# Performance work log

Hardware: AMD Instinct MI355X
Metric: run time of the kernel (lower is better)

The kernel has to match this reference:

```python
import jax, jax.numpy as jnp
import numpy as np

IN_F, OUT_F, HID_UNITS = 768, 4, 2048
H = (HID_UNITS // 16) * OUT_F          # 512
H_STANCE, OUT_S = 1024, 4
T, BR, L = 64, 4, 6                    # trees, branching factor, levels


def _build_forest():
    counts = np.array([BR ** (L - 1 - o) for o in range(L)])   # nodes per level, leaves (order 0) first
    starts = np.concatenate([[0], np.cumsum(counts)[:-1]])
    npt = int(counts.sum())                                    # 1365 nodes per tree
    offsets = np.arange(T) * npt
    node_order = np.tile(np.repeat(np.arange(L), counts), T)
    adj, eord = [], []
    for o in range(1, L):
        p = starts[o] + np.repeat(np.arange(counts[o]), BR)    # parents sorted, BR children each
        ch = starts[o - 1] + np.arange(counts[o - 1])
        pg = (offsets[:, None] + p[None, :]).reshape(-1)       # globally sorted parents per level
        cg = (offsets[:, None] + ch[None, :]).reshape(-1)
        adj.append(np.stack([pg, cg], 1))
        eord.append(np.full(pg.shape[0], o))
    return (node_order.astype(np.int32),
            np.concatenate(adj, 0).astype(np.int32),
            np.concatenate(eord).astype(np.int32),
            (offsets + starts[L - 1]).astype(np.int32),
            T * npt)


def setup_inputs():
    node_order, adjacency_list, edge_order, root_node, N = _build_forest()
    key = jax.random.key(0)
    ks = jax.random.split(key, 10)

    def xav(k, shape):
        lim = float(np.sqrt(6.0 / (shape[0] + shape[1])))
        return jax.random.uniform(k, shape, jnp.float32, -lim, lim)

    return {
        "features": jax.random.normal(ks[0], (N, IN_F), jnp.float32),
        "node_order": jnp.asarray(node_order),
        "adjacency_list": jnp.asarray(adjacency_list),
        "edge_order": jnp.asarray(edge_order),
        "root_node": jnp.asarray(root_node),
        "root_label": jax.random.randint(ks[1], (T,), 0, OUT_F, jnp.int32),
        "W_iou": xav(ks[2], (3 * H, IN_F)),
        "b_iou": jnp.zeros((3 * H,), jnp.float32),
        "U_iou": xav(ks[3], (3 * H, H)),
        "W_f": xav(ks[4], (H, IN_F)),
        "b_f": jnp.zeros((H,), jnp.float32),
        "U_f": xav(ks[5], (H, H)),
        "W_ff": xav(ks[6], (OUT_F, H)),
        "W_sd": xav(ks[7], (H_STANCE, H)),
        "W_sd2": xav(ks[8], (H, H_STANCE)),
        "W_sf": xav(ks[9], (OUT_S, H)),
        "ln_gamma": jnp.ones((OUT_S,), jnp.float32),
        "ln_beta": jnp.zeros((OUT_S,), jnp.float32),
    }


def _tree_lstm(features, node_order, adjacency_list, edge_order, root_node,
               W_iou, b_iou, U_iou, W_f, b_f, U_f,
               W_ff, W_sd, W_sd2, W_sf, ln_gamma, ln_beta):
    node_order = np.asarray(node_order)
    edge_order = np.asarray(edge_order)
    adjacency_list = np.asarray(adjacency_list)
    root_node = np.asarray(root_node)
    N = features.shape[0]
    Hd = W_f.shape[0]
    h = jnp.zeros((N, Hd), features.dtype)
    c = jnp.zeros((N, Hd), features.dtype)
    for n in range(int(node_order.max()) + 1):
        idx = np.nonzero(node_order == n)[0]           # nodes evaluated at this level (sorted)
        x = features[idx]
        if n == 0:
            iou = x @ W_iou.T + b_iou
            i, o, u = jnp.split(iou, 3, axis=1)
            c_new = jax.nn.sigmoid(i) * jnp.tanh(u)
        else:
            e = adjacency_list[edge_order == n]
            par, chi = e[:, 0], e[:, 1]                # parents grouped + sorted (unique_consecutive)
            seg = np.searchsorted(idx, par)            # parent id -> row within this level's block
            child_h = h[chi]
            child_c = c[chi]
            h_sum = jax.ops.segment_sum(child_h, seg, num_segments=idx.shape[0])
            iou = x @ W_iou.T + b_iou + h_sum @ U_iou.T
            i, o, u = jnp.split(iou, 3, axis=1)
            f = jax.nn.sigmoid(features[par] @ W_f.T + b_f + child_h @ U_f.T)
            c_sum = jax.ops.segment_sum(f * child_c, seg, num_segments=idx.shape[0])
            c_new = jax.nn.sigmoid(i) * jnp.tanh(u) + c_sum
        h_new = jax.nn.sigmoid(o) * jnp.tanh(c_new)
        c = c.at[idx].set(c_new)
        h = h.at[idx].set(h_new)
    residual = h
    h_root = h[root_node] @ W_ff.T
    h_st = (h @ W_sd.T) @ W_sd2.T + residual           # dropout = identity (eval mode)
    h_st = h_st @ W_sf.T
    mu = jnp.mean(h_st, axis=-1, keepdims=True)
    var = jnp.var(h_st, axis=-1, keepdims=True)
    h_st = (h_st - mu) * jax.lax.rsqrt(var + 1e-6) * ln_gamma + ln_beta
    return jax.nn.softmax(h_st, axis=1), jax.nn.softmax(h_root, axis=1), c


def reference(features, node_order, adjacency_list, edge_order, root_node, root_label,
              W_iou, b_iou, U_iou, W_f, b_f, U_f, W_ff, W_sd, W_sd2, W_sf, ln_gamma, ln_beta):
    return _tree_lstm(features, node_order, adjacency_list, edge_order, root_node,
                      W_iou, b_iou, U_iou, W_f, b_f, U_f,
                      W_ff, W_sd, W_sd2, W_sf, ln_gamma, ln_beta)
```

## Files before the change

kernel.cpp:

```cpp
#include <hip/hip_runtime.h>
#include <hip/hip_bf16.h>
#include <math.h>

typedef _Float16 f16;
typedef f16 f16x8 __attribute__((ext_vector_type(8)));
typedef float f32x4 __attribute__((ext_vector_type(4)));

#define NPT 1365
#define HD 512
#define NINT 341
#define IOU_LDS (2*128*64*2 + 2*192*64*2)
#define G128_LDS (2*128*64*2 + 2*128*64*2)

__device__ __forceinline__ float frcp(float x){ return __builtin_amdgcn_rcpf(x); }
__device__ __forceinline__ float sigm(float x){ return frcp(1.0f+__expf(-x)); }
__device__ __forceinline__ float ftanh(float x){
  float e=__expf(2.f*fabsf(x));
  float t=1.f-2.f*frcp(e+1.f);
  return copysignf(t,x);
}

__device__ __forceinline__ void gll16(const void* g, void* l){
  __builtin_amdgcn_global_load_lds((const __attribute__((address_space(1))) void*)g,
                                   (__attribute__((address_space(3))) void*)l, 16, 0, 0);
}

__device__ __forceinline__ void xcd_map(int phys, int nb, int xdim, int& x, int& my){
  int ytiles = nb / xdim;
  if((ytiles & 7)==0){
    int k = phys & 7, i = phys >> 3;
    my = k * (ytiles >> 3) + i / xdim;
    x  = i % xdim;
  }else{
    x  = phys % xdim;
    my = phys / xdim;
  }
}

__global__ void k_cvt16(const float* __restrict__ s, f16* __restrict__ d, size_t n8){
  size_t i=(size_t)blockIdx.x*blockDim.x+threadIdx.x;
  if(i>=n8) return;
  const float4* sp=(const float4*)(s+i*8);
  float4 a=sp[0], b=sp[1];
  float v[8]={a.x,a.y,a.z,a.w,b.x,b.y,b.z,b.w};
  f16x8 h;
  #pragma unroll
  for(int e=0;e<8;++e) h[e]=(f16)v[e];
  *(f16x8*)(d+i*8)=h;
}

__global__ void k_wil(const float* __restrict__ W, const float* __restrict__ U,
                      f16* __restrict__ d, int internal){
  const int K = internal? 1280 : 768;
  size_t i=(size_t)blockIdx.x*blockDim.x+threadIdx.x;
  size_t tot=(size_t)1536*K;
  if(i>=tot) return;
  int rp=(int)(i/K); int k=(int)(i-(size_t)rp*K);
  int f=rp>>4, rr=rp&15;
  int g=f%3, cgrp=f/3;
  int orig=g*512+cgrp*16+rr;
  float v;
  if(internal) v = (k<768)? W[(size_t)orig*768+k] : U[(size_t)orig*512+(k-768)];
  else         v = W[(size_t)orig*768+k];
  d[i]=(f16)v;
}

__global__ void k_concat1280(const float* __restrict__ W, const float* __restrict__ U,
                             f16* __restrict__ d, int rows){
  size_t i=(size_t)blockIdx.x*blockDim.x+threadIdx.x;
  const int K=1280;
  size_t tot=(size_t)rows*K;
  if(i>=tot) return;
  int r=(int)(i/K); int k=(int)(i-(size_t)r*K);
  float v = (k<768)? W[(size_t)r*768+k] : U[(size_t)r*512+(k-768)];
  d[i]=(f16)v;
}

__global__ void k_tmp4(const float* __restrict__ Wsf, const float* __restrict__ Wsd2,
                       float* __restrict__ tmp){
  int idx=blockIdx.x*256+threadIdx.x;
  if(idx>=4096) return;
  int j=idx>>10, e=idx&1023;
  float s=0.f;
  #pragma unroll 8
  for(int d=0;d<512;++d) s+=Wsf[j*512+d]*Wsd2[(size_t)d*1024+e];
  tmp[(size_t)j*1024+e]=s;
}

__global__ void k_wy2(const float* __restrict__ Wsf, const float* __restrict__ tmp,
                      const float* __restrict__ Wsd, float* __restrict__ Wy){
  int idx=blockIdx.x*256+threadIdx.x;
  if(idx>=2048) return;
  int j=idx>>9, c=idx&511;
  float s=Wsf[j*512+c];
  #pragma unroll 8
  for(int e=0;e<1024;++e) s+=tmp[j*1024+e]*Wsd[(size_t)e*512+c];
  Wy[(size_t)j*512+c]=s;
}

__global__ __launch_bounds__(256,2)
void k_iou128p(const f16* __restrict__ fx, const f16* __restrict__ hs16,
               const f16* __restrict__ Wil, const float* __restrict__ bias,
               const float* __restrict__ csum, f16* __restrict__ h16,
               float* __restrict__ cbuf,
               int start_n, int shift, int internal)
{
  extern __shared__ char sm[];
  char* Abase=sm;
  char* Bbase=sm+32768;
  const int tid=threadIdx.x;
  const int w=tid>>6, lane=tid&63;
  int x, my;
  xcd_map(blockIdx.x, gridDim.x, 8, x, my);
  const int m0=my*128;
  const int K = internal? 1280 : 768;
  const int NT = K>>6;

  unsigned fofs[4], hofs[4];
  #pragma unroll
  for(int i=0;i<4;++i){
    int r=w*32+i*8+(lane>>3);
    int m=m0+r;
    int t_=m>>shift, j=m-(t_<<shift);
    fofs[i]=(unsigned)(((size_t)t_*NPT+start_n+j)*768);
    hofs[i]=(unsigned)m*512u;
  }
  unsigned bofs[6];
  #pragma unroll
  for(int i=0;i<6;++i){
    int r=x*192+w*48+i*8+(lane>>3);
    bofs[i]=(unsigned)r*(unsigned)K;
  }
  const unsigned swz=8u*((unsigned)(lane&7)^(unsigned)(lane>>3));

  f32x4 acc[4][6];
  #pragma unroll
  for(int mi=0;mi<4;++mi)
    #pragma unroll
    for(int ni=0;ni<6;++ni) acc[mi][ni]=(f32x4){0.f,0.f,0.f,0.f};

  const int wr=(w>>1)*64;
  const int wcF=(w&1)*6;
  const int lr=lane&15, lg=lane>>4;

  auto STAGE=[&](int buf, int t){
    const f16* base; int kt; bool useF;
    if(internal){
      if(t<12){ base=fx;   kt=t;    useF=true;  }
      else    { base=hs16; kt=t-12; useF=false; }
    }else{
      base=fx; kt=t; useF=true;
    }
    const unsigned kofs=(unsigned)kt*64u+swz;
    char* Ad=Abase+(size_t)buf*16384;
    #pragma unroll
    for(int i=0;i<4;++i){
      const f16* g=base+(useF?fofs[i]:hofs[i])+kofs;
      gll16(g, Ad+(w*32+i*8)*128);
    }
    const unsigned bk=(unsigned)t*64u+swz;
    char* Bd=Bbase+(size_t)buf*24576;
    #pragma unroll
    for(int i=0;i<6;++i){
      gll16(Wil+bofs[i]+bk, Bd+(w*48+i*8)*128);
    }
  };

  auto COMPUTE=[&](int cur){
    const char* Ab=Abase+(size_t)cur*16384;
    const char* Bb=Bbase+(size_t)cur*24576;
    #pragma unroll
    for(int ks=0;ks<2;++ks){
      const unsigned cb=((unsigned)(ks*64+lg*16)) ^ ((unsigned)(lr&7)<<4);
      f16x8 av[4], bv[6];
      #pragma unroll
      for(int mi=0;mi<4;++mi)
        av[mi]=*(const f16x8*)(Ab+(unsigned)(wr+mi*16+lr)*128u+cb);
      #pragma unroll
      for(int ni=0;ni<6;++ni)
        bv[ni]=*(const f16x8*)(Bb+(unsigned)((wcF+ni)*16+lr)*128u+cb);
      __builtin_amdgcn_s_setprio(1);
      #pragma unroll
      for(int ni=0;ni<6;++ni)
        #pragma unroll
        for(int mi=0;mi<4;++mi)
          acc[mi][ni]=__builtin_amdgcn_mfma_f32_16x16x32_f16(av[mi],bv[ni],acc[mi][ni],0,0,0);
      __builtin_amdgcn_s_setprio(0);
    }
  };

  STAGE(0,0);
  STAGE(1,1);
  asm volatile("s_waitcnt vmcnt(10)" ::: "memory");
  __builtin_amdgcn_s_barrier();
  __builtin_amdgcn_sched_barrier(0);

  for(int t=0;t<NT;++t){
    COMPUTE(t&1);
    if(t+1<NT){
      __builtin_amdgcn_sched_barrier(0);
      __builtin_amdgcn_s_barrier();
      __builtin_amdgcn_sched_barrier(0);
      if(t+2<NT){
        STAGE(t&1, t+2);
        asm volatile("s_waitcnt vmcnt(10)" ::: "memory");
      }else{
        asm volatile("s_waitcnt vmcnt(0)" ::: "memory");
      }
      __builtin_amdgcn_s_barrier();
      __builtin_amdgcn_sched_barrier(0);
    }
  }

  #pragma unroll
  for(int mi=0;mi<4;++mi){
    #pragma unroll
    for(int cg=0;cg<2;++cg){
      const int col = x*64 + ((w&1)*2+cg)*16 + lr;
      const float bi=bias[col], bo=bias[col+512], bu=bias[col+1024];
      #pragma unroll
      for(int r=0;r<4;++r){
        const int mm=m0+wr+mi*16+lg*4+r;
        float iv=acc[mi][3*cg+0][r]+bi;
        float ov=acc[mi][3*cg+1][r]+bo;
        float uv=acc[mi][3*cg+2][r]+bu;
        float cn=sigm(iv)*ftanh(uv);
        if(internal) cn+=csum[(size_t)mm*HD+col];
        float hn=sigm(ov)*ftanh(cn);
        const int tt=mm>>shift, jj=mm-(tt<<shift);
        const size_t nd=((size_t)tt*NPT+start_n+jj)*HD+col;
        cbuf[nd]=cn;
        h16[nd]=(f16)hn;
      }
    }
  }
}

__global__ __launch_bounds__(256)
void k_iou(const f16* __restrict__ fx, const f16* __restrict__ hs16,
           const f16* __restrict__ Wcat, const float* __restrict__ bias,
           const float* __restrict__ csum, f16* __restrict__ h16,
           float* __restrict__ cbuf,
           int start_n, int shift, int K, int KB, int internal)
{
  __shared__ f16 As[64][40];
  __shared__ f16 Bs[3][64][40];
  const int tid=threadIdx.x;
  const int m0=blockIdx.x*64, n0=blockIdx.y*64;
  const int srow=tid>>2, skc=(tid&3)*8;
  const int m=m0+srow;
  const int t=m>>shift, j=m-(t<<shift);
  const size_t frow=((size_t)t*NPT+start_n+j)*768;
  const f16* aF=fx+frow;
  const f16* aH=hs16+(size_t)m*HD;
  const f16* bp0=Wcat+(size_t)(n0+srow)*KB;
  const f16* bp1=Wcat+(size_t)(512+n0+srow)*KB;
  const f16* bp2=Wcat+(size_t)(1024+n0+srow)*KB;

  f32x4 acc[3][2][2];
  #pragma unroll
  for(int g=0;g<3;++g)
    #pragma unroll
    for(int mi=0;mi<2;++mi)
      #pragma unroll
      for(int ni=0;ni<2;++ni) acc[g][mi][ni]=(f32x4){0.f,0.f,0.f,0.f};

  const int w=tid>>6, lane=tid&63;
  const int wr=(w>>1)*32, wc=(w&1)*32;
  const int lr=lane&15, lg=lane>>4;

  for(int k0=0;k0<K;k0+=32){
    const f16* ap = (k0<768)? (aF+k0) : (aH+(k0-768));
    *(f16x8*)&As[srow][skc]=*(const f16x8*)(ap+skc);
    *(f16x8*)&Bs[0][srow][skc]=*(const f16x8*)(bp0+k0+skc);
    *(f16x8*)&Bs[1][srow][skc]=*(const f16x8*)(bp1+k0+skc);
    *(f16x8*)&Bs[2][srow][skc]=*(const f16x8*)(bp2+k0+skc);
    __syncthreads();
    f16x8 a0=*(f16x8*)&As[wr+lr][lg*8];
    f16x8 a1=*(f16x8*)&As[wr+16+lr][lg*8];
    #pragma unroll
    for(int g=0;g<3;++g){
      #pragma unroll
      for(int ni=0;ni<2;++ni){
        f16x8 bv=*(f16x8*)&Bs[g][wc+ni*16+lr][lg*8];
        acc[g][0][ni]=__builtin_amdgcn_mfma_f32_16x16x32_f16(a0,bv,acc[g][0][ni],0,0,0);
        acc[g][1][ni]=__builtin_amdgcn_mfma_f32_16x16x32_f16(a1,bv,acc[g][1][ni],0,0,0);
      }
    }
    __syncthreads();
  }

  #pragma unroll
  for(int mi=0;mi<2;++mi){
    #pragma unroll
    for(int ni=0;ni<2;++ni){
      const int col=n0+wc+ni*16+lr;
      const float bi=bias[col], bo=bias[col+512], bu=bias[col+1024];
      #pragma unroll
      for(int r=0;r<4;++r){
        const int mm=m0+wr+mi*16+lg*4+r;
        float iv=acc[0][mi][ni][r]+bi;
        float ov=acc[1][mi][ni][r]+bo;
        float uv=acc[2][mi][ni][r]+bu;
        float cn=sigm(iv)*ftanh(uv);
        if(internal) cn+=csum[(size_t)mm*HD+col];
        float hn=sigm(ov)*ftanh(cn);
        const int tt=mm>>shift, jj=mm-(tt<<shift);
        const size_t nd=((size_t)tt*NPT+start_n+jj)*HD+col;
        cbuf[nd]=cn;
        h16[nd]=(f16)hn;
      }
    }
  }
}

__global__ __launch_bounds__(256,2)
void k_xwf128p(const f16* __restrict__ fx,
               const f16* __restrict__ Wfc, float* __restrict__ XWf, int Mtot)
{
  extern __shared__ char sm[];
  char* Abase=sm;
  char* Bbase=sm+32768;
  const int tid=threadIdx.x;
  const int w=tid>>6, lane=tid&63;
  int xb, my;
  xcd_map(blockIdx.x, gridDim.x, 4, xb, my);
  const int m0=my*128, n0=xb*128;
  const int NT=12;

  unsigned fofs[4];
  #pragma unroll
  for(int i=0;i<4;++i){
    int r=w*32+i*8+(lane>>3);
    int m=m0+r; if(m>=Mtot) m=Mtot-1;
    int t=m/NINT; int j=1024+(m-t*NINT);
    fofs[i]=(unsigned)(((size_t)t*NPT+j)*768);
  }
  unsigned bofs[4];
  #pragma unroll
  for(int i=0;i<4;++i){
    int r=n0+w*32+i*8+(lane>>3);
    bofs[i]=(unsigned)r*768u;
  }
  const unsigned swz=8u*((unsigned)(lane&7)^(unsigned)(lane>>3));

  f32x4 acc[4][4];
  #pragma unroll
  for(int mi=0;mi<4;++mi)
    #pragma unroll
    for(int ni=0;ni<4;++ni) acc[mi][ni]=(f32x4){0.f,0.f,0.f,0.f};

  const int wr=(w>>1)*64, wc=(w&1)*64;
  const int lr=lane&15, lg=lane>>4;

  auto STAGE=[&](int buf, int t){
    const unsigned ak=(unsigned)t*64u, bk=(unsigned)t*64u;
    char* Ad=Abase+(size_t)buf*16384;
    #pragma unroll
    for(int i=0;i<4;++i)
      gll16(fx+fofs[i]+ak+swz, Ad+(w*32+i*8)*128);
    char* Bd=Bbase+(size_t)buf*16384;
    #pragma unroll
    for(int i=0;i<4;++i)
      gll16(Wfc+bofs[i]+bk+swz, Bd+(w*32+i*8)*128);
  };

  auto COMPUTE=[&](int cur){
    const char* Ab=Abase+(size_t)cur*16384;
    const char* Bb=Bbase+(size_t)cur*16384;
    #pragma unroll
    for(int ks=0;ks<2;++ks){
      const unsigned cb=((unsigned)(ks*64+lg*16)) ^ ((unsigned)(lr&7)<<4);
      f16x8 av[4], bv[4];
      #pragma unroll
      for(int mi=0;mi<4;++mi)
        av[mi]=*(const f16x8*)(Ab+(unsigned)(wr+mi*16+lr)*128u+cb);
      #pragma unroll
      for(int ni=0;ni<4;++ni)
        bv[ni]=*(const f16x8*)(Bb+(unsigned)((wc+ni*16)+lr)*128u+cb);
      __builtin_amdgcn_s_setprio(1);
      #pragma unroll
      for(int ni=0;ni<4;++ni)
        #pragma unroll
        for(int mi=0;mi<4;++mi)
          acc[mi][ni]=__builtin_amdgcn_mfma_f32_16x16x32_f16(av[mi],bv[ni],acc[mi][ni],0,0,0);
      __builtin_amdgcn_s_setprio(0);
    }
  };

  STAGE(0,0);
  STAGE(1,1);
  asm volatile("s_waitcnt vmcnt(8)" ::: "memory");
  __builtin_amdgcn_s_barrier();
  __builtin_amdgcn_sched_barrier(0);

  for(int t=0;t<NT;++t){
    COMPUTE(t&1);
    if(t+1<NT){
      __builtin_amdgcn_sched_barrier(0);
      __builtin_amdgcn_s_barrier();
      __builtin_amdgcn_sched_barrier(0);
      if(t+2<NT){
        STAGE(t&1, t+2);
        asm volatile("s_waitcnt vmcnt(8)" ::: "memory");
      }else{
        asm volatile("s_waitcnt vmcnt(0)" ::: "memory");
      }
      __builtin_amdgcn_s_barrier();
      __builtin_amdgcn_sched_barrier(0);
    }
  }

  #pragma unroll
  for(int mi=0;mi<4;++mi){
    #pragma unroll
    for(int ni=0;ni<4;++ni){
      const int col=n0+wc+ni*16+lr;
      #pragma unroll
      for(int r=0;r<4;++r){
        const int mm=m0+wr+mi*16+lg*4+r;
        if(mm<Mtot) XWf[(size_t)mm*512+col]=acc[mi][ni][r];
      }
    }
  }
}

__global__ __launch_bounds__(256,2)
void k_uh128p(const f16* __restrict__ h16,
              const f16* __restrict__ Ufc, const float* __restrict__ bias,
              const float* __restrict__ XWf, const float* __restrict__ cbuf,
              float* __restrict__ csum, f16* __restrict__ hs16,
              int start_ch, int lc, int xwoff)
{
  extern __shared__ char sm[];
  char* Abase=sm;
  char* Bbase=sm+32768;
  const int tid=threadIdx.x;
  const int w=tid>>6, lane=tid&63;
  int xb, my;
  xcd_map(blockIdx.x, gridDim.x, 4, xb, my);
  const int e0=my*128, n0=xb*128;
  const int NT=8;

  unsigned hofs[4];
  #pragma unroll
  for(int i=0;i<4;++i){
    int r=w*32+i*8+(lane>>3);
    int e=e0+r;
    int t=e>>lc, ei=e-(t<<lc);
    hofs[i]=(unsigned)(((size_t)t*NPT+start_ch+ei)*HD);
  }
  unsigned bofs[4];
  #pragma unroll
  for(int i=0;i<4;++i){
    int r=n0+w*32+i*8+(lane>>3);
    bofs[i]=(unsigned)r*512u;
  }
  const unsigned swz=8u*((unsigned)(lane&7)^(unsigned)(lane>>3));

  f32x4 acc[4][4];
  #pragma unroll
  for(int mi=0;mi<4;++mi)
    #pragma unroll
    for(int ni=0;ni<4;++ni) acc[mi][ni]=(f32x4){0.f,0.f,0.f,0.f};

  const int wr=(w>>1)*64, wc=(w&1)*64;
  const int lr=lane&15, lg=lane>>4;

  auto STAGE=[&](int buf, int t){
    const unsigned ak=(unsigned)t*64u, bk=(unsigned)t*64u;
    char* Ad=Abase+(size_t)buf*16384;
    #pragma unroll
    for(int i=0;i<4;++i)
      gll16(h16+hofs[i]+ak+swz, Ad+(w*32+i*8)*128);
    char* Bd=Bbase+(size_t)buf*16384;
    #pragma unroll
    for(int i=0;i<4;++i)
      gll16(Ufc+bofs[i]+bk+swz, Bd+(w*32+i*8)*128);
  };

  auto COMPUTE=[&](int cur){
    const char* Ab=Abase+(size_t)cur*16384;
    const char* Bb=Bbase+(size_t)cur*16384;
    #pragma unroll
    for(int ks=0;ks<2;++ks){
      const unsigned cb=((unsigned)(ks*64+lg*16)) ^ ((unsigned)(lr&7)<<4);
      f16x8 av[4], bv[4];
      #pragma unroll
      for(int mi=0;mi<4;++mi)
        av[mi]=*(const f16x8*)(Ab+(unsigned)(wr+mi*16+lr)*128u+cb);
      #pragma unroll
      for(int ni=0;ni<4;++ni)
        bv[ni]=*(const f16x8*)(Bb+(unsigned)((wc+ni*16)+lr)*128u+cb);
      __builtin_amdgcn_s_setprio(1);
      #pragma unroll
      for(int ni=0;ni<4;++ni)
        #pragma unroll
        for(int mi=0;mi<4;++mi)
          acc[mi][ni]=__builtin_amdgcn_mfma_f32_16x16x32_f16(av[mi],bv[ni],acc[mi][ni],0,0,0);
      __builtin_amdgcn_s_setprio(0);
    }
  };

  STAGE(0,0);
  STAGE(1,1);
  asm volatile("s_waitcnt vmcnt(8)" ::: "memory");
  __builtin_amdgcn_s_barrier();
  __builtin_amdgcn_sched_barrier(0);

  for(int t=0;t<NT;++t){
    COMPUTE(t&1);
    if(t+1<NT){
      __builtin_amdgcn_sched_barrier(0);
      __builtin_amdgcn_s_barrier();
      __builtin_amdgcn_sched_barrier(0);
      if(t+2<NT){
        STAGE(t&1, t+2);
        asm volatile("s_waitcnt vmcnt(8)" ::: "memory");
      }else{
        asm volatile("s_waitcnt vmcnt(0)" ::: "memory");
      }
      __builtin_amdgcn_s_barrier();
      __builtin_amdgcn_sched_barrier(0);
    }
  }

  #pragma unroll
  for(int mi=0;mi<4;++mi){
    const int ebase=e0+wr+mi*16+lg*4;
    const int tt=ebase>>lc, eib=ebase-(tt<<lc);
    const int inode=tt*NINT + xwoff + (eib>>2);
    const int par=ebase>>2;
    #pragma unroll
    for(int ni=0;ni<4;++ni){
      const int col=n0+wc+ni*16+lr;
      const float base=bias[col]+XWf[(size_t)inode*512+col];
      const size_t chbase=((size_t)tt*NPT+start_ch+eib)*HD+col;
      float s=0.f, hsv=0.f;
      #pragma unroll
      for(int r=0;r<4;++r){
        const size_t ci=chbase+(size_t)r*HD;
        float fv=sigm(acc[mi][ni][r]+base);
        s+=fv*cbuf[ci];
        hsv+=(float)h16[ci];
      }
      csum[(size_t)par*HD+col]=s;
      hs16[(size_t)par*HD+col]=(f16)hsv;
    }
  }
}

__global__ __launch_bounds__(256)
void k_final2(const f16* __restrict__ h16,
              const float* __restrict__ Wy, const float* __restrict__ gamma,
              const float* __restrict__ beta, float* __restrict__ out0, int Nn)
{
  const int gtid=blockIdx.x*256+threadIdx.x;
  const int node=gtid>>6, lane=gtid&63;
  if(node>=Nn) return;
  const size_t base=(size_t)node*HD+lane*8;
  f16x8 hv=*(const f16x8*)(h16+base);
  float hf[8];
  #pragma unroll
  for(int e=0;e<8;++e) hf[e]=(float)hv[e];
  float y[4];
  #pragma unroll
  for(int jj=0;jj<4;++jj){
    const float* wp=Wy+jj*HD+lane*8;
    float s=0.f;
    #pragma unroll
    for(int e=0;e<8;++e) s+=hf[e]*wp[e];
    #pragma unroll
    for(int off=32;off>=1;off>>=1) s+=__shfl_xor(s,off,64);
    y[jj]=s;
  }
  if(lane==0){
    float mu=0.25f*(y[0]+y[1]+y[2]+y[3]);
    float var=0.f;
    #pragma unroll
    for(int jj=0;jj<4;++jj){ float d=y[jj]-mu; var+=d*d; }
    var*=0.25f;
    float rs=rsqrtf(var+1e-6f);
    float z[4], zmax=-1e30f;
    #pragma unroll
    for(int jj=0;jj<4;++jj){ z[jj]=(y[jj]-mu)*rs*gamma[jj]+beta[jj]; zmax=fmaxf(zmax,z[jj]); }
    float es=0.f;
    #pragma unroll
    for(int jj=0;jj<4;++jj){ z[jj]=__expf(z[jj]-zmax); es+=z[jj]; }
    float inv=1.f/es;
    #pragma unroll
    for(int jj=0;jj<4;++jj) out0[(size_t)node*4+jj]=z[jj]*inv;
  }
}

__global__ __launch_bounds__(256)
void k_root(const f16* __restrict__ h16,
            const float* __restrict__ Wff, float* __restrict__ out1)
{
  const int gtid=blockIdx.x*256+threadIdx.x;
  const int tt=gtid>>6, lane=gtid&63;
  if(tt>=64) return;
  const size_t base=((size_t)tt*NPT+1364)*HD+lane*8;
  f16x8 hv=*(const f16x8*)(h16+base);
  float hf[8];
  #pragma unroll
  for(int e=0;e<8;++e) hf[e]=(float)hv[e];
  float y[4];
  #pragma unroll
  for(int jj=0;jj<4;++jj){
    const float* wp=Wff+jj*HD+lane*8;
    float s=0.f;
    #pragma unroll
    for(int e=0;e<8;++e) s+=hf[e]*wp[e];
    #pragma unroll
    for(int off=32;off>=1;off>>=1) s+=__shfl_xor(s,off,64);
    y[jj]=s;
  }
  if(lane==0){
    float zmax=fmaxf(fmaxf(y[0],y[1]),fmaxf(y[2],y[3]));
    float es=0.f, z[4];
    #pragma unroll
    for(int jj=0;jj<4;++jj){ z[jj]=__expf(y[jj]-zmax); es+=z[jj]; }
    float inv=1.f/es;
    #pragma unroll
    for(int jj=0;jj<4;++jj) out1[(size_t)tt*4+jj]=z[jj]*inv;
  }
}

extern "C" void kernel_launch(void* const* d_in, const int* in_sizes, int n_in,
                              void* d_out, int out_size, void* d_ws, size_t ws_size,
                              hipStream_t stream)
{
  const float* features=(const float*)d_in[0];
  const float* W_iou=(const float*)d_in[6];
  const float* b_iou=(const float*)d_in[7];
  const float* U_iou=(const float*)d_in[8];
  const float* W_f  =(const float*)d_in[9];
  const float* b_f  =(const float*)d_in[10];
  const float* U_f  =(const float*)d_in[11];
  const float* W_ff =(const float*)d_in[12];
  const float* W_sd =(const float*)d_in[13];
  const float* W_sd2=(const float*)d_in[14];
  const float* W_sf =(const float*)d_in[15];
  const float* ln_g =(const float*)d_in[16];
  const float* ln_b =(const float*)d_in[17];

  const int N=in_sizes[0]/768;
  const int T=N/NPT;
  const int MINT=T*NINT;

  float* out0=(float*)d_out;
  float* out1=out0+(size_t)N*4;
  float* cbuf=out1+(size_t)T*4;

  char* p=(char*)d_ws;
  auto alloc=[&](size_t bytes){ char* r=p; p+=((bytes+255)&~(size_t)255); return r; };
  f16*   fx   =(f16*)  alloc((size_t)N*768*2);
  f16*   hs16 =(f16*)  alloc((size_t)16384*HD*2);
  float* csum =(float*)alloc((size_t)16384*HD*4);
  f16*   h16  =(f16*)  alloc((size_t)N*HD*2);
  f16*   WilL =(f16*)  alloc((size_t)1536*768*2);
  f16*   WilI =(f16*)  alloc((size_t)1536*1280*2);
  f16*   Wcat2=(f16*)  alloc((size_t)1536*1280*2);
  f16*   Wfc  =(f16*)  alloc((size_t)512*768*2);
  f16*   Ufc  =(f16*)  alloc((size_t)512*512*2);
  float* tmp4 =(float*)alloc((size_t)4*1024*4);
  float* Wy   =(float*)alloc((size_t)4*512*4);
  float* XWf  =(float*)alloc((size_t)MINT*512*4);

  { size_t n8=(size_t)N*768/8;    k_cvt16<<<(int)((n8+255)/256),256,0,stream>>>(features,fx,n8); }
  { size_t n=(size_t)1536*768;    k_wil<<<(int)((n+255)/256),256,0,stream>>>(W_iou,U_iou,WilL,0); }
  { size_t n=(size_t)1536*1280;   k_wil<<<(int)((n+255)/256),256,0,stream>>>(W_iou,U_iou,WilI,1); }
  { size_t n=(size_t)1536*1280;   k_concat1280<<<(int)((n+255)/256),256,0,stream>>>(W_iou,U_iou,Wcat2,1536); }
  { size_t n8=(size_t)512*768/8;  k_cvt16<<<(int)((n8+255)/256),256,0,stream>>>(W_f,Wfc,n8); }
  { size_t n8=(size_t)512*512/8;  k_cvt16<<<(int)((n8+255)/256),256,0,stream>>>(U_f,Ufc,n8); }
  { k_tmp4<<<16,256,0,stream>>>(W_sf,W_sd2,tmp4); }
  { k_wy2<<<8,256,0,stream>>>(W_sf,tmp4,W_sd,Wy); }

  { int nb=4*((MINT+127)/128);
    k_xwf128p<<<nb,256,G128_LDS,stream>>>(fx,Wfc,XWf,MINT); }

  static const int starts[6]={0,1024,1280,1344,1360,1364};
  static const int csh[6]  ={10,8,6,4,2,0};
  static const int counts[6]={1024,256,64,16,4,1};
  static const int xwoffs[6]={0,0,256,320,336,340};

  { int nb=8*((T*1024)/128);
    k_iou128p<<<nb,256,IOU_LDS,stream>>>(fx,hs16,WilL,b_iou,csum,h16,cbuf,0,10,0); }

  for(int n=1;n<6;++n){
    int P=T*counts[n], E=T*counts[n-1];
    { int nb=4*(E/128);
      k_uh128p<<<nb,256,G128_LDS,stream>>>(h16,Ufc,b_f,XWf,cbuf,csum,hs16,
                                           starts[n-1],csh[n-1],xwoffs[n]); }
    if(P>=128){
      int nb=8*(P/128);
      k_iou128p<<<nb,256,IOU_LDS,stream>>>(fx,hs16,WilI,b_iou,csum,h16,cbuf,starts[n],csh[n],1);
    }else{
      dim3 g(P/64,8);
      k_iou<<<g,256,0,stream>>>(fx,hs16,Wcat2,b_iou,csum,h16,cbuf,starts[n],csh[n],1280,1280,1);
    }
  }

  { int th=N*64; k_final2<<<(th+255)/256,256,0,stream>>>(h16,Wy,ln_g,ln_b,out0,N); }
  { k_root<<<16,256,0,stream>>>(h16,W_ff,out1); }
}
```

Baseline: 807.8 us.

## Merge prep kernels, fuse leaf IOU with XWf GEMM, and fuse final/root kernels

Collapses the seven weight/feature conversion kernels into a single multi-range prep kernel. The leaf-level IOU GEMM and the internal-node W_f projection GEMM now run as one launch, with blocks split by index. The final LayerNorm/softmax and root softmax kernels are merged into one launch. The goal is fewer kernel launches and serialization gaps, and letting the two independent GEMMs share the GPU. In exchange, the fused kernels carry more branching, and the prep kernel mixes heavy tmp4 dot-product threads with cheap conversion threads.

```diff
diff --git a/kernel.cpp b/kernel.cpp
--- a/kernel.cpp
+++ b/kernel.cpp
@@ -37,54 +37,75 @@
   }
 }
 
-__global__ void k_cvt16(const float* __restrict__ s, f16* __restrict__ d, size_t n8){
-  size_t i=(size_t)blockIdx.x*blockDim.x+threadIdx.x;
-  if(i>=n8) return;
-  const float4* sp=(const float4*)(s+i*8);
-  float4 a=sp[0], b=sp[1];
-  float v[8]={a.x,a.y,a.z,a.w,b.x,b.y,b.z,b.w};
-  f16x8 h;
-  #pragma unroll
-  for(int e=0;e<8;++e) h[e]=(f16)v[e];
-  *(f16x8*)(d+i*8)=h;
-}
-
-__global__ void k_wil(const float* __restrict__ W, const float* __restrict__ U,
-                      f16* __restrict__ d, int internal){
-  const int K = internal? 1280 : 768;
-  size_t i=(size_t)blockIdx.x*blockDim.x+threadIdx.x;
-  size_t tot=(size_t)1536*K;
-  if(i>=tot) return;
-  int rp=(int)(i/K); int k=(int)(i-(size_t)rp*K);
-  int f=rp>>4, rr=rp&15;
-  int g=f%3, cgrp=f/3;
-  int orig=g*512+cgrp*16+rr;
-  float v;
-  if(internal) v = (k<768)? W[(size_t)orig*768+k] : U[(size_t)orig*512+(k-768)];
-  else         v = W[(size_t)orig*768+k];
-  d[i]=(f16)v;
-}
-
-__global__ void k_concat1280(const float* __restrict__ W, const float* __restrict__ U,
-                             f16* __restrict__ d, int rows){
-  size_t i=(size_t)blockIdx.x*blockDim.x+threadIdx.x;
-  const int K=1280;
-  size_t tot=(size_t)rows*K;
-  if(i>=tot) return;
-  int r=(int)(i/K); int k=(int)(i-(size_t)r*K);
-  float v = (k<768)? W[(size_t)r*768+k] : U[(size_t)r*512+(k-768)];
-  d[i]=(f16)v;
-}
-
-__global__ void k_tmp4(const float* __restrict__ Wsf, const float* __restrict__ Wsd2,
-                       float* __restrict__ tmp){
-  int idx=blockIdx.x*256+threadIdx.x;
-  if(idx>=4096) return;
-  int j=idx>>10, e=idx&1023;
-  float s=0.f;
-  #pragma unroll 8
-  for(int d=0;d<512;++d) s+=Wsf[j*512+d]*Wsd2[(size_t)d*1024+e];
-  tmp[(size_t)j*1024+e]=s;
+__global__ void k_prep(const float* __restrict__ features,
+                       const float* __restrict__ W_iou, const float* __restrict__ U_iou,
+                       const float* __restrict__ W_f, const float* __restrict__ U_f,
+                       const float* __restrict__ Wsf, const float* __restrict__ Wsd2,
+                       f16* __restrict__ fx, f16* __restrict__ WilL, f16* __restrict__ WilI,
+                       f16* __restrict__ Wcat2, f16* __restrict__ Wfc, f16* __restrict__ Ufc,
+                       float* __restrict__ tmp4, size_t nfeat8)
+{
+  size_t gid=(size_t)blockIdx.x*256+threadIdx.x;
+  const size_t n0=nfeat8;
+  const size_t n1=n0+(size_t)1536*768;
+  const size_t n2=n1+(size_t)1536*1280;
+  const size_t n3=n2+(size_t)1536*1280;
+  const size_t n4=n3+(size_t)512*768/8;
+  const size_t n5=n4+(size_t)512*512/8;
+  const size_t n6=n5+4096;
+  if(gid<n0){
+    size_t i=gid;
+    const float4* sp=(const float4*)(features+i*8);
+    float4 a=sp[0], b=sp[1];
+    float v[8]={a.x,a.y,a.z,a.w,b.x,b.y,b.z,b.w};
+    f16x8 h;
+    #pragma unroll
+    for(int e=0;e<8;++e) h[e]=(f16)v[e];
+    *(f16x8*)(fx+i*8)=h;
+  }else if(gid<n1){
+    size_t i=gid-n0;
+    int rp=(int)(i/768); int k=(int)(i-(size_t)rp*768);
+    int f=rp>>4, rr=rp&15;
+    int orig=(f%3)*512+(f/3)*16+rr;
+    WilL[i]=(f16)W_iou[(size_t)orig*768+k];
+  }else if(gid<n2){
+    size_t i=gid-n1;
+    int rp=(int)(i/1280); int k=(int)(i-(size_t)rp*1280);
+    int f=rp>>4, rr=rp&15;
+    int orig=(f%3)*512+(f/3)*16+rr;
+    float v=(k<768)? W_iou[(size_t)orig*768+k] : U_iou[(size_t)orig*512+(k-768)];
+    WilI[i]=(f16)v;
+  }else if(gid<n3){
+    size_t i=gid-n2;
+    int r=(int)(i/1280); int k=(int)(i-(size_t)r*1280);
+    float v=(k<768)? W_iou[(size_t)r*768+k] : U_iou[(size_t)r*512+(k-768)];
+    Wcat2[i]=(f16)v;
+  }else if(gid<n4){
+    size_t i=gid-n3;
+    const float4* sp=(const float4*)(W_f+i*8);
+    float4 a=sp[0], b=sp[1];
+    float v[8]={a.x,a.y,a.z,a.w,b.x,b.y,b.z,b.w};
+    f16x8 h;
+    #pragma unroll
+    for(int e=0;e<8;++e) h[e]=(f16)v[e];
+    *(f16x8*)(Wfc+i*8)=h;
+  }else if(gid<n5){
+    size_t i=gid-n4;
+    const float4* sp=(const float4*)(U_f+i*8);
+    float4 a=sp[0], b=sp[1];
+    float v[8]={a.x,a.y,a.z,a.w,b.x,b.y,b.z,b.w};
+    f16x8 h;
+    #pragma unroll
+    for(int e=0;e<8;++e) h[e]=(f16)v[e];
+    *(f16x8*)(Ufc+i*8)=h;
+  }else if(gid<n6){
+    int idx=(int)(gid-n5);
+    int j=idx>>10, e=idx&1023;
+    float s=0.f;
+    #pragma unroll 8
+    for(int d=0;d<512;++d) s+=Wsf[j*512+d]*Wsd2[(size_t)d*1024+e];
+    tmp4[(size_t)j*1024+e]=s;
+  }
 }
 
 __global__ void k_wy2(const float* __restrict__ Wsf, const float* __restrict__ tmp,
@@ -99,11 +120,241 @@
 }
 
 __global__ __launch_bounds__(256,2)
+void k_leafxwf(const f16* __restrict__ fx, const f16* __restrict__ WilL,
+               const float* __restrict__ bias, f16* __restrict__ h16,
+               float* __restrict__ cbuf,
+               const f16* __restrict__ Wfc, float* __restrict__ XWf,
+               int nbLeaf, int Mtot)
+{
+  extern __shared__ char sm[];
+  const int tid=threadIdx.x;
+  const int w=tid>>6, lane=tid&63;
+  const int lr=lane&15, lg=lane>>4;
+  const unsigned swz=8u*((unsigned)(lane&7)^(unsigned)(lane>>3));
+
+  if((int)blockIdx.x < nbLeaf){
+    char* Abase=sm;
+    char* Bbase=sm+32768;
+    int x, my;
+    xcd_map(blockIdx.x, nbLeaf, 8, x, my);
+    const int m0=my*128;
+    const int NT=12;
+
+    unsigned fofs[4];
+    #pragma unroll
+    for(int i=0;i<4;++i){
+      int r=w*32+i*8+(lane>>3);
+      int m=m0+r;
+      int t_=m>>10, j=m-(t_<<10);
+      fofs[i]=(unsigned)(((size_t)t_*NPT+j)*768);
+    }
+    unsigned bofs[6];
+    #pragma unroll
+    for(int i=0;i<6;++i){
+      int r=x*192+w*48+i*8+(lane>>3);
+      bofs[i]=(unsigned)r*768u;
+    }
+
+    f32x4 acc[4][6];
+    #pragma unroll
+    for(int mi=0;mi<4;++mi)
+      #pragma unroll
+      for(int ni=0;ni<6;++ni) acc[mi][ni]=(f32x4){0.f,0.f,0.f,0.f};
+
+    const int wr=(w>>1)*64;
+    const int wcF=(w&1)*6;
+
+    auto STAGE=[&](int buf, int t){
+      const unsigned kofs=(unsigned)t*64u+swz;
+      char* Ad=Abase+(size_t)buf*16384;
+      #pragma unroll
+      for(int i=0;i<4;++i)
+        gll16(fx+fofs[i]+kofs, Ad+(w*32+i*8)*128);
+      char* Bd=Bbase+(size_t)buf*24576;
+      #pragma unroll
+      for(int i=0;i<6;++i)
+        gll16(WilL+bofs[i]+kofs, Bd+(w*48+i*8)*128);
+    };
+
+    auto COMPUTE=[&](int cur){
+      const char* Ab=Abase+(size_t)cur*16384;
+      const char* Bb=Bbase+(size_t)cur*24576;
+      #pragma unroll
+      for(int ks=0;ks<2;++ks){
+        const unsigned cb=((unsigned)(ks*64+lg*16)) ^ ((unsigned)(lr&7)<<4);
+        f16x8 av[4], bv[6];
+        #pragma unroll
+        for(int mi=0;mi<4;++mi)
+          av[mi]=*(const f16x8*)(Ab+(unsigned)(wr+mi*16+lr)*128u+cb);
+        #pragma unroll
+        for(int ni=0;ni<6;++ni)
+          bv[ni]=*(const f16x8*)(Bb+(unsigned)((wcF+ni)*16+lr)*128u+cb);
+        __builtin_amdgcn_s_setprio(1);
+        #pragma unroll
+        for(int ni=0;ni<6;++ni)
+          #pragma unroll
+          for(int mi=0;mi<4;++mi)
+            acc[mi][ni]=__builtin_amdgcn_mfma_f32_16x16x32_f16(av[mi],bv[ni],acc[mi][ni],0,0,0);
+        __builtin_amdgcn_s_setprio(0);
+      }
+    };
+
+    STAGE(0,0);
+    STAGE(1,1);
+    asm volatile("s_waitcnt vmcnt(10)" ::: "memory");
+    __builtin_amdgcn_s_barrier();
+    __builtin_amdgcn_sched_barrier(0);
+
+    for(int t=0;t<NT;++t){
+      COMPUTE(t&1);
+      if(t+1<NT){
+        __builtin_amdgcn_sched_barrier(0);
+        __builtin_amdgcn_s_barrier();
+        __builtin_amdgcn_sched_barrier(0);
+        if(t+2<NT){
+          STAGE(t&1, t+2);
+          asm volatile("s_waitcnt vmcnt(10)" ::: "memory");
+        }else{
+          asm volatile("s_waitcnt vmcnt(0)" ::: "memory");
+        }
+        __builtin_amdgcn_s_barrier();
+        __builtin_amdgcn_sched_barrier(0);
+      }
+    }
+
+    #pragma unroll
+    for(int mi=0;mi<4;++mi){
+      #pragma unroll
+      for(int cg=0;cg<2;++cg){
+        const int col = x*64 + ((w&1)*2+cg)*16 + lr;
+        const float bi=bias[col], bo=bias[col+512], bu=bias[col+1024];
+        #pragma unroll
+        for(int r=0;r<4;++r){
+          const int mm=m0+wr+mi*16+lg*4+r;
+          float iv=acc[mi][3*cg+0][r]+bi;
+          float ov=acc[mi][3*cg+1][r]+bo;
+          float uv=acc[mi][3*cg+2][r]+bu;
+          float cn=sigm(iv)*ftanh(uv);
+          float hn=sigm(ov)*ftanh(cn);
+          const int tt=mm>>10, jj=mm-(tt<<10);
+          const size_t nd=((size_t)tt*NPT+jj)*HD+col;
+          cbuf[nd]=cn;
+          h16[nd]=(f16)hn;
+        }
+      }
+    }
+  } else {
+    char* Abase=sm;
+    char* Bbase=sm+32768;
+    int phys=(int)blockIdx.x-nbLeaf;
+    int nb=(int)gridDim.x-nbLeaf;
+    int xb, my;
+    xcd_map(phys, nb, 4, xb, my);
+    const int m0=my*128, n0=xb*128;
+    const int NT=12;
+
+    unsigned fofs[4];
+    #pragma unroll
+    for(int i=0;i<4;++i){
+      int r=w*32+i*8+(lane>>3);
+      int m=m0+r; if(m>=Mtot) m=Mtot-1;
+      int t=m/NINT; int j=1024+(m-t*NINT);
+      fofs[i]=(unsigned)(((size_t)t*NPT+j)*768);
+    }
+    unsigned bofs[4];
+    #pragma unroll
+    for(int i=0;i<4;++i){
+      int r=n0+w*32+i*8+(lane>>3);
+      bofs[i]=(unsigned)r*768u;
+    }
+
+    f32x4 acc[4][4];
+    #pragma unroll
+    for(int mi=0;mi<4;++mi)
+      #pragma unroll
+      for(int ni=0;ni<4;++ni) acc[mi][ni]=(f32x4){0.f,0.f,0.f,0.f};
+
+    const int wr=(w>>1)*64, wc=(w&1)*64;
+
+    auto STAGE=[&](int buf, int t){
+      const unsigned ak=(unsigned)t*64u+swz;
+      char* Ad=Abase+(size_t)buf*16384;
+      #pragma unroll
+      for(int i=0;i<4;++i)
+        gll16(fx+fofs[i]+ak, Ad+(w*32+i*8)*128);
+      char* Bd=Bbase+(size_t)buf*16384;
+      #pragma unroll
+      for(int i=0;i<4;++i)
+        gll16(Wfc+bofs[i]+ak, Bd+(w*32+i*8)*128);
+    };
+
+    auto COMPUTE=[&](int cur){
+      const char* Ab=Abase+(size_t)cur*16384;
+      const char* Bb=Bbase+(size_t)cur*16384;
+      #pragma unroll
+      for(int ks=0;ks<2;++ks){
+        const unsigned cb=((unsigned)(ks*64+lg*16)) ^ ((unsigned)(lr&7)<<4);
+        f16x8 av[4], bv[4];
+        #pragma unroll
+        for(int mi=0;mi<4;++mi)
+          av[mi]=*(const f16x8*)(Ab+(unsigned)(wr+mi*16+lr)*128u+cb);
+        #pragma unroll
+        for(int ni=0;ni<4;++ni)
+          bv[ni]=*(const f16x8*)(Bb+(unsigned)((wc+ni*16)+lr)*128u+cb);
+        __builtin_amdgcn_s_setprio(1);
+        #pragma unroll
+        for(int ni=0;ni<4;++ni)
+          #pragma unroll
+          for(int mi=0;mi<4;++mi)
+            acc[mi][ni]=__builtin_amdgcn_mfma_f32_16x16x32_f16(av[mi],bv[ni],acc[mi][ni],0,0,0);
+        __builtin_amdgcn_s_setprio(0);
+      }
+    };
+
+    STAGE(0,0);
+    STAGE(1,1);
+    asm volatile("s_waitcnt vmcnt(8)" ::: "memory");
+    __builtin_amdgcn_s_barrier();
+    __builtin_amdgcn_sched_barrier(0);
+
+    for(int t=0;t<NT;++t){
+      COMPUTE(t&1);
+      if(t+1<NT){
+        __builtin_amdgcn_sched_barrier(0);
+        __builtin_amdgcn_s_barrier();
+        __builtin_amdgcn_sched_barrier(0);
+        if(t+2<NT){
+          STAGE(t&1, t+2);
+          asm volatile("s_waitcnt vmcnt(8)" ::: "memory");
+        }else{
+          asm volatile("s_waitcnt vmcnt(0)" ::: "memory");
+        }
+        __builtin_amdgcn_s_barrier();
+        __builtin_amdgcn_sched_barrier(0);
+      }
+    }
+
+    #pragma unroll
+    for(int mi=0;mi<4;++mi){
+      #pragma unroll
+      for(int ni=0;ni<4;++ni){
+        const int col=n0+wc+ni*16+lr;
+        #pragma unroll
+        for(int r=0;r<4;++r){
+          const int mm=m0+wr+mi*16+lg*4+r;
+          if(mm<Mtot) XWf[(size_t)mm*512+col]=acc[mi][ni][r];
+        }
+      }
+    }
+  }
+}
+
+__global__ __launch_bounds__(256,2)
 void k_iou128p(const f16* __restrict__ fx, const f16* __restrict__ hs16,
                const f16* __restrict__ Wil, const float* __restrict__ bias,
                const float* __restrict__ csum, f16* __restrict__ h16,
                float* __restrict__ cbuf,
-               int start_n, int shift, int internal)
+               int start_n, int shift)
 {
   extern __shared__ char sm[];
   char* Abase=sm;
@@ -113,8 +364,8 @@
   int x, my;
   xcd_map(blockIdx.x, gridDim.x, 8, x, my);
   const int m0=my*128;
-  const int K = internal? 1280 : 768;
-  const int NT = K>>6;
+  const int K=1280;
+  const int NT=20;
 
   unsigned fofs[4], hofs[4];
   #pragma unroll
@@ -145,12 +396,8 @@
 
   auto STAGE=[&](int buf, int t){
     const f16* base; int kt; bool useF;
-    if(internal){
-      if(t<12){ base=fx;   kt=t;    useF=true;  }
-      else    { base=hs16; kt=t-12; useF=false; }
-    }else{
-      base=fx; kt=t; useF=true;
-    }
+    if(t<12){ base=fx;   kt=t;    useF=true;  }
+    else    { base=hs16; kt=t-12; useF=false; }
     const unsigned kofs=(unsigned)kt*64u+swz;
     char* Ad=Abase+(size_t)buf*16384;
     #pragma unroll
@@ -225,7 +472,7 @@
         float ov=acc[mi][3*cg+1][r]+bo;
         float uv=acc[mi][3*cg+2][r]+bu;
         float cn=sigm(iv)*ftanh(uv);
-        if(internal) cn+=csum[(size_t)mm*HD+col];
+        cn+=csum[(size_t)mm*HD+col];
         float hn=sigm(ov)*ftanh(cn);
         const int tt=mm>>shift, jj=mm-(tt<<shift);
         const size_t nd=((size_t)tt*NPT+start_n+jj)*HD+col;
@@ -241,7 +488,7 @@
            const f16* __restrict__ Wcat, const float* __restrict__ bias,
            const float* __restrict__ csum, f16* __restrict__ h16,
            float* __restrict__ cbuf,
-           int start_n, int shift, int K, int KB, int internal)
+           int start_n, int shift, int K, int KB)
 {
   __shared__ f16 As[64][40];
   __shared__ f16 Bs[3][64][40];
@@ -303,123 +550,12 @@
         float ov=acc[1][mi][ni][r]+bo;
         float uv=acc[2][mi][ni][r]+bu;
         float cn=sigm(iv)*ftanh(uv);
-        if(internal) cn+=csum[(size_t)mm*HD+col];
+        cn+=csum[(size_t)mm*HD+col];
         float hn=sigm(ov)*ftanh(cn);
         const int tt=mm>>shift, jj=mm-(tt<<shift);
         const size_t nd=((size_t)tt*NPT+start_n+jj)*HD+col;
         cbuf[nd]=cn;
         h16[nd]=(f16)hn;
-      }
-    }
-  }
-}
-
-__global__ __launch_bounds__(256,2)
-void k_xwf128p(const f16* __restrict__ fx,
-               const f16* __restrict__ Wfc, float* __restrict__ XWf, int Mtot)
-{
-  extern __shared__ char sm[];
-  char* Abase=sm;
-  char* Bbase=sm+32768;
-  const int tid=threadIdx.x;
-  const int w=tid>>6, lane=tid&63;
-  int xb, my;
-  xcd_map(blockIdx.x, gridDim.x, 4, xb, my);
-  const int m0=my*128, n0=xb*128;
-  const int NT=12;
-
-  unsigned fofs[4];
-  #pragma unroll
-  for(int i=0;i<4;++i){
-    int r=w*32+i*8+(lane>>3);
-    int m=m0+r; if(m>=Mtot) m=Mtot-1;
-    int t=m/NINT; int j=1024+(m-t*NINT);
-    fofs[i]=(unsigned)(((size_t)t*NPT+j)*768);
-  }
-  unsigned bofs[4];
-  #pragma unroll
-  for(int i=0;i<4;++i){
-    int r=n0+w*32+i*8+(lane>>3);
-    bofs[i]=(unsigned)r*768u;
-  }
-  const unsigned swz=8u*((unsigned)(lane&7)^(unsigned)(lane>>3));
-
-  f32x4 acc[4][4];
-  #pragma unroll
-  for(int mi=0;mi<4;++mi)
-    #pragma unroll
-    for(int ni=0;ni<4;++ni) acc[mi][ni]=(f32x4){0.f,0.f,0.f,0.f};
-
-  const int wr=(w>>1)*64, wc=(w&1)*64;
-  const int lr=lane&15, lg=lane>>4;
-
-  auto STAGE=[&](int buf, int t){
-    const unsigned ak=(unsigned)t*64u, bk=(unsigned)t*64u;
-    char* Ad=Abase+(size_t)buf*16384;
-    #pragma unroll
-    for(int i=0;i<4;++i)
-      gll16(fx+fofs[i]+ak+swz, Ad+(w*32+i*8)*128);
-    char* Bd=Bbase+(size_t)buf*16384;
-    #pragma unroll
-    for(int i=0;i<4;++i)
-      gll16(Wfc+bofs[i]+bk+swz, Bd+(w*32+i*8)*128);
-  };
-
-  auto COMPUTE=[&](int cur){
-    const char* Ab=Abase+(size_t)cur*16384;
-    const char* Bb=Bbase+(size_t)cur*16384;
-    #pragma unroll
-    for(int ks=0;ks<2;++ks){
-      const unsigned cb=((unsigned)(ks*64+lg*16)) ^ ((unsigned)(lr&7)<<4);
-      f16x8 av[4], bv[4];
-      #pragma unroll
-      for(int mi=0;mi<4;++mi)
-        av[mi]=*(const f16x8*)(Ab+(unsigned)(wr+mi*16+lr)*128u+cb);
-      #pragma unroll
-      for(int ni=0;ni<4;++ni)
-        bv[ni]=*(const f16x8*)(Bb+(unsigned)((wc+ni*16)+lr)*128u+cb);
-      __builtin_amdgcn_s_setprio(1);
-      #pragma unroll
-      for(int ni=0;ni<4;++ni)
-        #pragma unroll
-        for(int mi=0;mi<4;++mi)
-          acc[mi][ni]=__builtin_amdgcn_mfma_f32_16x16x32_f16(av[mi],bv[ni],acc[mi][ni],0,0,0);
-      __builtin_amdgcn_s_setprio(0);
-    }
-  };
-
-  STAGE(0,0);
-  STAGE(1,1);
-  asm volatile("s_waitcnt vmcnt(8)" ::: "memory");
-  __builtin_amdgcn_s_barrier();
-  __builtin_amdgcn_sched_barrier(0);
-
-  for(int t=0;t<NT;++t){
-    COMPUTE(t&1);
-    if(t+1<NT){
-      __builtin_amdgcn_sched_barrier(0);
-      __builtin_amdgcn_s_barrier();
-      __builtin_amdgcn_sched_barrier(0);
-      if(t+2<NT){
-        STAGE(t&1, t+2);
-        asm volatile("s_waitcnt vmcnt(8)" ::: "memory");
-      }else{
-        asm volatile("s_waitcnt vmcnt(0)" ::: "memory");
-      }
-      __builtin_amdgcn_s_barrier();
-      __builtin_amdgcn_sched_barrier(0);
-    }
-  }
-
-  #pragma unroll
-  for(int mi=0;mi<4;++mi){
-    #pragma unroll
-    for(int ni=0;ni<4;++ni){
-      const int col=n0+wc+ni*16+lr;
-      #pragma unroll
-      for(int r=0;r<4;++r){
-        const int mm=m0+wr+mi*16+lg*4+r;
-        if(mm<Mtot) XWf[(size_t)mm*512+col]=acc[mi][ni][r];
       }
     }
   }
@@ -468,15 +604,15 @@
   const int lr=lane&15, lg=lane>>4;
 
   auto STAGE=[&](int buf, int t){
-    const unsigned ak=(unsigned)t*64u, bk=(unsigned)t*64u;
+    const unsigned ak=(unsigned)t*64u+swz;
     char* Ad=Abase+(size_t)buf*16384;
     #pragma unroll
     for(int i=0;i<4;++i)
-      gll16(h16+hofs[i]+ak+swz, Ad+(w*32+i*8)*128);
+      gll16(h16+hofs[i]+ak, Ad+(w*32+i*8)*128);
     char* Bd=Bbase+(size_t)buf*16384;
     #pragma unroll
     for(int i=0;i<4;++i)
-      gll16(Ufc+bofs[i]+bk+swz, Bd+(w*32+i*8)*128);
+      gll16(Ufc+bofs[i]+ak, Bd+(w*32+i*8)*128);
   };
 
   auto COMPUTE=[&](int cur){
@@ -553,77 +689,77 @@
 __global__ __launch_bounds__(256)
 void k_final2(const f16* __restrict__ h16,
               const float* __restrict__ Wy, const float* __restrict__ gamma,
-              const float* __restrict__ beta, float* __restrict__ out0, int Nn)
+              const float* __restrict__ beta, float* __restrict__ out0,
+              const float* __restrict__ Wff, float* __restrict__ out1,
+              int Nn, int nbMain)
 {
-  const int gtid=blockIdx.x*256+threadIdx.x;
-  const int node=gtid>>6, lane=gtid&63;
-  if(node>=Nn) return;
-  const size_t base=(size_t)node*HD+lane*8;
-  f16x8 hv=*(const f16x8*)(h16+base);
-  float hf[8];
-  #pragma unroll
-  for(int e=0;e<8;++e) hf[e]=(float)hv[e];
-  float y[4];
-  #pragma unroll
-  for(int jj=0;jj<4;++jj){
-    const float* wp=Wy+jj*HD+lane*8;
-    float s=0.f;
-    #pragma unroll
-    for(int e=0;e<8;++e) s+=hf[e]*wp[e];
-    #pragma unroll
-    for(int off=32;off>=1;off>>=1) s+=__shfl_xor(s,off,64);
-    y[jj]=s;
-  }
-  if(lane==0){
-    float mu=0.25f*(y[0]+y[1]+y[2]+y[3]);
-    float var=0.f;
-    #pragma unroll
-    for(int jj=0;jj<4;++jj){ float d=y[jj]-mu; var+=d*d; }
-    var*=0.25f;
-    float rs=rsqrtf(var+1e-6f);
-    float z[4], zmax=-1e30f;
-    #pragma unroll
-    for(int jj=0;jj<4;++jj){ z[jj]=(y[jj]-mu)*rs*gamma[jj]+beta[jj]; zmax=fmaxf(zmax,z[jj]); }
-    float es=0.f;
-    #pragma unroll
-    for(int jj=0;jj<4;++jj){ z[jj]=__expf(z[jj]-zmax); es+=z[jj]; }
-    float inv=1.f/es;
-    #pragma unroll
-    for(int jj=0;jj<4;++jj) out0[(size_t)node*4+jj]=z[jj]*inv;
-  }
-}
-
-__global__ __launch_bounds__(256)
-void k_root(const f16* __restrict__ h16,
-            const float* __restrict__ Wff, float* __restrict__ out1)
-{
-  const int gtid=blockIdx.x*256+threadIdx.x;
-  const int tt=gtid>>6, lane=gtid&63;
-  if(tt>=64) return;
-  const size_t base=((size_t)tt*NPT+1364)*HD+lane*8;
-  f16x8 hv=*(const f16x8*)(h16+base);
-  float hf[8];
-  #pragma unroll
-  for(int e=0;e<8;++e) hf[e]=(float)hv[e];
-  float y[4];
-  #pragma unroll
-  for(int jj=0;jj<4;++jj){
-    const float* wp=Wff+jj*HD+lane*8;
-    float s=0.f;
-    #pragma unroll
-    for(int e=0;e<8;++e) s+=hf[e]*wp[e];
-    #pragma unroll
-    for(int off=32;off>=1;off>>=1) s+=__shfl_xor(s,off,64);
-    y[jj]=s;
-  }
-  if(lane==0){
-    float zmax=fmaxf(fmaxf(y[0],y[1]),fmaxf(y[2],y[3]));
-    float es=0.f, z[4];
-    #pragma unroll
-    for(int jj=0;jj<4;++jj){ z[jj]=__expf(y[jj]-zmax); es+=z[jj]; }
-    float inv=1.f/es;
-    #pragma unroll
-    for(int jj=0;jj<4;++jj) out1[(size_t)tt*4+jj]=z[jj]*inv;
+  const int tid=threadIdx.x;
+  if((int)blockIdx.x < nbMain){
+    const int gtid=blockIdx.x*256+tid;
+    const int node=gtid>>6, lane=gtid&63;
+    if(node>=Nn) return;
+    const size_t base=(size_t)node*HD+lane*8;
+    f16x8 hv=*(const f16x8*)(h16+base);
+    float hf[8];
+    #pragma unroll
+    for(int e=0;e<8;++e) hf[e]=(float)hv[e];
+    float y[4];
+    #pragma unroll
+    for(int jj=0;jj<4;++jj){
+      const float* wp=Wy+jj*HD+lane*8;
+      float s=0.f;
+      #pragma unroll
+      for(int e=0;e<8;++e) s+=hf[e]*wp[e];
+      #pragma unroll
+      for(int off=32;off>=1;off>>=1) s+=__shfl_xor(s,off,64);
+      y[jj]=s;
+    }
+    if(lane==0){
+      float mu=0.25f*(y[0]+y[1]+y[2]+y[3]);
+      float var=0.f;
+      #pragma unroll
+      for(int jj=0;jj<4;++jj){ float d=y[jj]-mu; var+=d*d; }
+      var*=0.25f;
+      float rs=rsqrtf(var+1e-6f);
+      float z[4], zmax=-1e30f;
+      #pragma unroll
+      for(int jj=0;jj<4;++jj){ z[jj]=(y[jj]-mu)*rs*gamma[jj]+beta[jj]; zmax=fmaxf(zmax,z[jj]); }
+      float es=0.f;
+      #pragma unroll
+      for(int jj=0;jj<4;++jj){ z[jj]=__expf(z[jj]-zmax); es+=z[jj]; }
+      float inv=frcp(es);
+      #pragma unroll
+      for(int jj=0;jj<4;++jj) out0[(size_t)node*4+jj]=z[jj]*inv;
+    }
+  } else {
+    const int gtid=((int)blockIdx.x-nbMain)*256+tid;
+    const int tt=gtid>>6, lane=gtid&63;
+    if(tt>=64) return;
+    const size_t base=((size_t)tt*NPT+1364)*HD+lane*8;
+    f16x8 hv=*(const f16x8*)(h16+base);
+    float hf[8];
+    #pragma unroll
+    for(int e=0;e<8;++e) hf[e]=(float)hv[e];
+    float y[4];
+    #pragma unroll
+    for(int jj=0;jj<4;++jj){
+      const float* wp=Wff+jj*HD+lane*8;
+      float s=0.f;
+      #pragma unroll
+      for(int e=0;e<8;++e) s+=hf[e]*wp[e];
+      #pragma unroll
+      for(int off=32;off>=1;off>>=1) s+=__shfl_xor(s,off,64);
+      y[jj]=s;
+    }
+    if(lane==0){
+      float zmax=fmaxf(fmaxf(y[0],y[1]),fmaxf(y[2],y[3]));
+      float es=0.f, z[4];
+      #pragma unroll
+      for(int jj=0;jj<4;++jj){ z[jj]=__expf(y[jj]-zmax); es+=z[jj]; }
+      float inv=frcp(es);
+      #pragma unroll
+      for(int jj=0;jj<4;++jj) out1[(size_t)tt*4+jj]=z[jj]*inv;
+    }
   }
 }
 
@@ -668,25 +804,25 @@
   float* Wy   =(float*)alloc((size_t)4*512*4);
   float* XWf  =(float*)alloc((size_t)MINT*512*4);
 
-  { size_t n8=(size_t)N*768/8;    k_cvt16<<<(int)((n8+255)/256),256,0,stream>>>(features,fx,n8); }
-  { size_t n=(size_t)1536*768;    k_wil<<<(int)((n+255)/256),256,0,stream>>>(W_iou,U_iou,WilL,0); }
-  { size_t n=(size_t)1536*1280;   k_wil<<<(int)((n+255)/256),256,0,stream>>>(W_iou,U_iou,WilI,1); }
-  { size_t n=(size_t)1536*1280;   k_concat1280<<<(int)((n+255)/256),256,0,stream>>>(W_iou,U_iou,Wcat2,1536); }
-  { size_t n8=(size_t)512*768/8;  k_cvt16<<<(int)((n8+255)/256),256,0,stream>>>(W_f,Wfc,n8); }
-  { size_t n8=(size_t)512*512/8;  k_cvt16<<<(int)((n8+255)/256),256,0,stream>>>(U_f,Ufc,n8); }
-  { k_tmp4<<<16,256,0,stream>>>(W_sf,W_sd2,tmp4); }
+  {
+    size_t nfeat8=(size_t)N*768/8;
+    size_t tot=nfeat8+(size_t)1536*768+(size_t)1536*1280*2+(size_t)512*768/8+(size_t)512*512/8+4096;
+    int nb=(int)((tot+255)/256);
+    k_prep<<<nb,256,0,stream>>>(features,W_iou,U_iou,W_f,U_f,W_sf,W_sd2,
+                                fx,WilL,WilI,Wcat2,Wfc,Ufc,tmp4,nfeat8);
+  }
   { k_wy2<<<8,256,0,stream>>>(W_sf,tmp4,W_sd,Wy); }
-
-  { int nb=4*((MINT+127)/128);
-    k_xwf128p<<<nb,256,G128_LDS,stream>>>(fx,Wfc,XWf,MINT); }
 
   static const int starts[6]={0,1024,1280,1344,1360,1364};
   static const int csh[6]  ={10,8,6,4,2,0};
   static const int counts[6]={1024,256,64,16,4,1};
   static const int xwoffs[6]={0,0,256,320,336,340};
 
-  { int nb=8*((T*1024)/128);
-    k_iou128p<<<nb,256,IOU_LDS,stream>>>(fx,hs16,WilL,b_iou,csum,h16,cbuf,0,10,0); }
+  {
+    int nbLeaf=8*((T*1024)/128);
+    int nbXwf=4*((MINT+127)/128);
+    k_leafxwf<<<nbLeaf+nbXwf,256,IOU_LDS,stream>>>(fx,WilL,b_iou,h16,cbuf,Wfc,XWf,nbLeaf,MINT);
+  }
 
   for(int n=1;n<6;++n){
     int P=T*counts[n], E=T*counts[n-1];
@@ -695,13 +831,15 @@
                                            starts[n-1],csh[n-1],xwoffs[n]); }
     if(P>=128){
       int nb=8*(P/128);
-      k_iou128p<<<nb,256,IOU_LDS,stream>>>(fx,hs16,WilI,b_iou,csum,h16,cbuf,starts[n],csh[n],1);
+      k_iou128p<<<nb,256,IOU_LDS,stream>>>(fx,hs16,WilI,b_iou,csum,h16,cbuf,starts[n],csh[n]);
     }else{
       dim3 g(P/64,8);
-      k_iou<<<g,256,0,stream>>>(fx,hs16,Wcat2,b_iou,csum,h16,cbuf,starts[n],csh[n],1280,1280,1);
-    }
-  }
-
-  { int th=N*64; k_final2<<<(th+255)/256,256,0,stream>>>(h16,Wy,ln_g,ln_b,out0,N); }
-  { k_root<<<16,256,0,stream>>>(h16,W_ff,out1); }
-}
+      k_iou<<<g,256,0,stream>>>(fx,hs16,Wcat2,b_iou,csum,h16,cbuf,starts[n],csh[n],1280,1280);
+    }
+  }
+
+  {
+    int nbMain=(N*64+255)/256;
+    k_final2<<<nbMain+16,256,0,stream>>>(h16,Wy,ln_g,ln_b,out0,W_ff,out1,N,nbMain);
+  }
+}
```

New measurement: 735.0 us (median of 2 runs). -9.0%, faster.
